# Kernel tuning notes

Measured on AMD Instinct MI355X. Metric: run time of the kernel, lower is better.

The kernel has to match this reference:

```python
import jax, jax.numpy as jnp
import numpy as np

R = 3.0            # search_range
EPS = 0.01         # forward_backward_error
UPD_MULT = 1.0     # UPDATE_MULTIPLIER_THRESHOLD


def _clamp(coords, H, W):
    # coords [..., 2] = (x, y); clamp x to [0, W-1], y to [0, H-1]
    return jnp.stack([jnp.clip(coords[..., 0], 0.0, W - 1.0),
                      jnp.clip(coords[..., 1], 0.0, H - 1.0)], axis=-1)


def _scores(coords, corr_flat):
    # coords [B,H,W,2] (x,y); corr_flat [B*H*W, Hc, Wc]; bilinear sample one scalar per pixel
    B, H, W, _ = coords.shape
    N, Hc, Wc = corr_flat.shape
    c = coords.reshape(-1, 2)
    x, y = c[:, 0], c[:, 1]
    x0 = jnp.floor(x); y0 = jnp.floor(y)
    wx = x - x0; wy = y - y0
    x0i = jnp.clip(x0.astype(jnp.int32), 0, Wc - 1)
    x1i = jnp.clip(x0i + 1, 0, Wc - 1)
    y0i = jnp.clip(y0.astype(jnp.int32), 0, Hc - 1)
    y1i = jnp.clip(y0i + 1, 0, Hc - 1)
    n = jnp.arange(N)
    v00 = corr_flat[n, y0i, x0i]; v01 = corr_flat[n, y0i, x1i]
    v10 = corr_flat[n, y1i, x0i]; v11 = corr_flat[n, y1i, x1i]
    s = (v00 * (1 - wx) * (1 - wy) + v01 * wx * (1 - wy)
         + v10 * (1 - wx) * wy + v11 * wx * wy)
    return s.reshape(B, H, W)


def _propagate(coords, corr_flat, dxy):
    # PatchMatch propagation step along direction (dx, dy): take neighbor's match
    # shifted by the same pixel offset if it scores higher.
    dx, dy = dxy
    B, H, W, _ = coords.shape
    best = coords
    best_s = _scores(best, corr_flat)
    cand_h = _clamp(jnp.roll(coords, dx, axis=2) + jnp.array([dx, 0.0], coords.dtype), H, W)
    cand_v = _clamp(jnp.roll(coords, dy, axis=1) + jnp.array([0.0, dy], coords.dtype), H, W)
    for cand in (cand_h, cand_v):
        s = _scores(cand, corr_flat)
        upd = s > best_s
        best = jnp.where(upd[..., None], cand, best)
        best_s = jnp.maximum(s, best_s)
    return best


def _random_search(coords, corr_flat, key):
    B, H, W, _ = coords.shape
    new = _clamp(coords + R * jax.random.normal(key, coords.shape, coords.dtype), H, W)
    old_s = _scores(coords, corr_flat)
    new_s = _scores(new, corr_flat)
    upd = (new_s - UPD_MULT * old_s) > 0
    return jnp.where(upd[..., None], new, coords)


def _handle(matching, corr_flat, key):
    coords = jnp.transpose(matching, (0, 2, 3, 1))  # [B,H,W,2]
    k1, k2, k3 = jax.random.split(key, 3)
    res = _propagate(coords, corr_flat, (1, 1))
    res = _random_search(res, corr_flat, k1)
    res = _propagate(res, corr_flat, (-1, -1))
    res = _random_search(res, corr_flat, k2)
    res = _propagate(res, corr_flat, (-1, 1))
    res = _random_search(res, corr_flat, k3)
    res = _propagate(res, corr_flat, (1, -1))
    return res


def _bilinear_map(img, coords):
    # img [B,H,W,C] sampled at coords [B,H,W,2] (x,y) -> [B,H,W,C]
    B, H, W, C = img.shape
    def per_b(im, co):
        x = co[..., 0].reshape(-1); y = co[..., 1].reshape(-1)
        x0 = jnp.floor(x); y0 = jnp.floor(y)
        wx = (x - x0)[:, None]; wy = (y - y0)[:, None]
        x0i = jnp.clip(x0.astype(jnp.int32), 0, W - 1)
        x1i = jnp.clip(x0i + 1, 0, W - 1)
        y0i = jnp.clip(y0.astype(jnp.int32), 0, H - 1)
        y1i = jnp.clip(y0i + 1, 0, H - 1)
        v00 = im[y0i, x0i]; v01 = im[y0i, x1i]
        v10 = im[y1i, x0i]; v11 = im[y1i, x1i]
        out = (v00 * (1 - wx) * (1 - wy) + v01 * wx * (1 - wy)
               + v10 * (1 - wx) * wy + v11 * wx * wy)
        return out.reshape(H, W, C)
    return jax.vmap(per_b)(img, coords)


def setup_inputs() -> dict:
    key = jax.random.key(0)
    k1, k2, k3 = jax.random.split(key, 3)
    B, H, W = 4, 64, 64
    # matching fields: absolute (x, y) coords in-range
    mf = jax.random.uniform(k1, (B, 2, H, W), jnp.float32)
    mb = jax.random.uniform(k2, (B, 2, H, W), jnp.float32)
    scale = jnp.array([W - 1.0, H - 1.0], jnp.float32).reshape(1, 2, 1, 1)
    matching_f = mf * scale
    matching_b = mb * scale
    corr_map = jax.random.normal(k3, (B, H, W, H, W), jnp.float32)
    return {"matching_f": matching_f, "matching_b": matching_b, "corr_map": corr_map}


def reference(matching_f, matching_b, corr_map):
    B, H, W = corr_map.shape[0], corr_map.shape[1], corr_map.shape[2]
    corr_f = corr_map.reshape(B * H * W, H, W)
    # backward direction samples the transposed correlation volume
    corr_b = jnp.transpose(corr_map, (0, 3, 4, 1, 2)).reshape(B * H * W, H, W)
    key = jax.random.key(42)
    kf, kb = jax.random.split(key)
    res_f = _handle(matching_f, corr_f, kf)   # [B,H,W,2]
    res_b = _handle(matching_b, corr_b, kb)   # [B,H,W,2]
    # forward-backward consistency: sample backward field at forward matches
    counter = _bilinear_map(res_b, res_f)
    diff = jnp.max(jnp.abs(res_f - counter), axis=-1)
    invalid = (diff > EPS)[..., None]
    res = jnp.where(invalid, jnp.transpose(matching_f, (0, 2, 3, 1)), res_f)
    return jnp.transpose(res, (0, 3, 1, 2))
```

## Files before the change

### kernel.cpp

```cpp
#include <hip/hip_runtime.h>
#include <stdint.h>

#pragma clang fp contract(off)

__host__ __device__ inline void tf2x32(uint32_t k0, uint32_t k1,
                                       uint32_t x0, uint32_t x1,
                                       uint32_t* o0, uint32_t* o1) {
  const uint32_t ks2 = k0 ^ k1 ^ 0x1BD11BDAu;
  x0 += k0; x1 += k1;
#define TF_R(r) { x0 += x1; x1 = (x1 << (r)) | (x1 >> (32 - (r))); x1 ^= x0; }
  TF_R(13) TF_R(15) TF_R(26) TF_R(6)
  x0 += k1;  x1 += ks2 + 1u;
  TF_R(17) TF_R(29) TF_R(16) TF_R(24)
  x0 += ks2; x1 += k0 + 2u;
  TF_R(13) TF_R(15) TF_R(26) TF_R(6)
  x0 += k0;  x1 += k1 + 3u;
  TF_R(17) TF_R(29) TF_R(16) TF_R(24)
  x0 += k1;  x1 += ks2 + 4u;
  TF_R(13) TF_R(15) TF_R(26) TF_R(6)
  x0 += ks2; x1 += k0 + 5u;
#undef TF_R
  *o0 = x0; *o1 = x1;
}

__device__ inline float erfinv_xla(float x) {
#pragma clang fp contract(off)
  float w = -log1pf(-(x * x));
  float p;
  if (w < 5.0f) {
    w = w - 2.5f;
    p = 2.81022636e-08f;
    p = 3.43273939e-07f  + p * w;
    p = -3.5233877e-06f  + p * w;
    p = -4.39150654e-06f + p * w;
    p = 0.00021858087f   + p * w;
    p = -0.00125372503f  + p * w;
    p = -0.00417768164f  + p * w;
    p = 0.246640727f     + p * w;
    p = 1.50140941f      + p * w;
  } else {
    w = sqrtf(w) - 3.0f;
    p = -0.000200214257f;
    p = 0.000100950558f  + p * w;
    p = 0.00134934322f   + p * w;
    p = -0.00367342844f  + p * w;
    p = 0.00573950773f   + p * w;
    p = -0.0076224613f   + p * w;
    p = 0.00943887047f   + p * w;
    p = 1.00167406f      + p * w;
    p = 2.83297682f      + p * w;
  }
  return p * x;
}

__device__ inline float jax_normal(uint32_t k0, uint32_t k1, uint32_t idx) {
#pragma clang fp contract(off)
  uint32_t o0, o1;
  tf2x32(k0, k1, 0u, idx, &o0, &o1);
  uint32_t bits = o0 ^ o1;
  float f = __uint_as_float((bits >> 9) | 0x3f800000u) - 1.0f;
  float u = f * 2.0f + (-0x1.fffffep-1f);
  u = fmaxf(-0x1.fffffep-1f, u);
  return 0x1.6a09e6p+0f * erfinv_xla(u);
}

__device__ inline float score_at(const float* __restrict__ base, int stride,
                                 float x, float y) {
#pragma clang fp contract(off)
  float x0 = floorf(x), y0 = floorf(y);
  float wx = x - x0, wy = y - y0;
  int xi = (int)x0; xi = xi < 0 ? 0 : (xi > 63 ? 63 : xi);
  int yi = (int)y0; yi = yi < 0 ? 0 : (yi > 63 ? 63 : yi);
  int x1 = xi + 1 > 63 ? 63 : xi + 1;
  int y1 = yi + 1 > 63 ? 63 : yi + 1;
  float v00 = base[(yi * 64 + xi) * stride];
  float v01 = base[(yi * 64 + x1) * stride];
  float v10 = base[(y1 * 64 + xi) * stride];
  float v11 = base[(y1 * 64 + x1) * stride];
  float omx = 1.0f - wx, omy = 1.0f - wy;
  return (((v00 * omx) * omy + (v01 * wx) * omy) + (v10 * omx) * wy) + (v11 * wx) * wy;
}

__global__ __launch_bounds__(64) void step_kernel(
    const float* __restrict__ mf, const float* __restrict__ mb,
    const float2* __restrict__ in_c, float2* __restrict__ out_c,
    const float* __restrict__ corr, int dx, int dy,
    uint32_t k0f, uint32_t k1f, uint32_t k0b, uint32_t k1b,
    int do_rs, int from_matching) {
#pragma clang fp contract(off)
  int g = (int)(blockIdx.x * 64 + threadIdx.x);
  int dir = g >> 14, b = (g >> 12) & 3, p = g & 4095;
  int i = p >> 6, j = p & 63;

  const float* base; int stride;
  if (dir == 0) { base = corr + (size_t)(b * 4096 + p) * 4096; stride = 1; }
  else          { base = corr + (size_t)b * 16777216 + p;      stride = 4096; }

  float2 c, ch, cv;
  int jh = (j - dx) & 63;
  int iv = (i - dy) & 63;
  if (from_matching) {
    const float* m = dir ? mb : mf;
    c  = make_float2(m[((b * 2 + 0) * 64 + i ) * 64 + j ], m[((b * 2 + 1) * 64 + i ) * 64 + j ]);
    ch = make_float2(m[((b * 2 + 0) * 64 + i ) * 64 + jh], m[((b * 2 + 1) * 64 + i ) * 64 + jh]);
    cv = make_float2(m[((b * 2 + 0) * 64 + iv) * 64 + j ], m[((b * 2 + 1) * 64 + iv) * 64 + j ]);
  } else {
    const float2* ic = in_c + dir * 16384 + b * 4096;
    c  = ic[p];
    ch = ic[(i << 6) | jh];
    cv = ic[(iv << 6) | j];
  }
  ch.x = fminf(fmaxf(ch.x + (float)dx, 0.0f), 63.0f);
  cv.y = fminf(fmaxf(cv.y + (float)dy, 0.0f), 63.0f);

  float s0 = score_at(base, stride, c.x,  c.y);
  float sh = score_at(base, stride, ch.x, ch.y);
  float sv = score_at(base, stride, cv.x, cv.y);
  float2 bst = c; float bs = s0;
  if (sh > bs) bst = ch;
  bs = fmaxf(sh, bs);
  if (sv > bs) bst = cv;
  bs = fmaxf(sv, bs);

  if (do_rs) {
    uint32_t kk0 = dir ? k0b : k0f, kk1 = dir ? k1b : k1f;
    uint32_t pg = (uint32_t)(b * 4096 + p);
    float n0 = jax_normal(kk0, kk1, 2u * pg);
    float n1 = jax_normal(kk0, kk1, 2u * pg + 1u);
    float nx = fminf(fmaxf(bst.x + 3.0f * n0, 0.0f), 63.0f);
    float ny = fminf(fmaxf(bst.y + 3.0f * n1, 0.0f), 63.0f);
    float sn = score_at(base, stride, nx, ny);
    if (sn - bs > 0.0f) bst = make_float2(nx, ny);
  }
  out_c[dir * 16384 + b * 4096 + p] = bst;
}

__global__ __launch_bounds__(256) void combine_kernel(const float* __restrict__ mf,
                                                      const float2* __restrict__ res,
                                                      float* __restrict__ out) {
#pragma clang fp contract(off)
  int pg = (int)(blockIdx.x * 256 + threadIdx.x);
  int b = pg >> 12, hw = pg & 4095;
  int i = hw >> 6, j = hw & 63;
  float2 rf = res[pg];
  const float2* rb = res + 16384 + b * 4096;
  float x0 = floorf(rf.x), y0 = floorf(rf.y);
  float wx = rf.x - x0, wy = rf.y - y0;
  int xi = (int)x0; xi = xi < 0 ? 0 : (xi > 63 ? 63 : xi);
  int yi = (int)y0; yi = yi < 0 ? 0 : (yi > 63 ? 63 : yi);
  int x1 = xi + 1 > 63 ? 63 : xi + 1;
  int y1 = yi + 1 > 63 ? 63 : yi + 1;
  float2 v00 = rb[yi * 64 + xi], v01 = rb[yi * 64 + x1];
  float2 v10 = rb[y1 * 64 + xi], v11 = rb[y1 * 64 + x1];
  float omx = 1.0f - wx, omy = 1.0f - wy;
  float c0 = (((v00.x * omx) * omy + (v01.x * wx) * omy) + (v10.x * omx) * wy) + (v11.x * wx) * wy;
  float c1 = (((v00.y * omx) * omy + (v01.y * wx) * omy) + (v10.y * omx) * wy) + (v11.y * wx) * wy;
  float d = fmaxf(fabsf(rf.x - c0), fabsf(rf.y - c1));
  bool invalid = d > 0.01f;
  out[((b * 2 + 0) * 64 + i) * 64 + j] = invalid ? mf[((b * 2 + 0) * 64 + i) * 64 + j] : rf.x;
  out[((b * 2 + 1) * 64 + i) * 64 + j] = invalid ? mf[((b * 2 + 1) * 64 + i) * 64 + j] : rf.y;
}

extern "C" void kernel_launch(void* const* d_in, const int* in_sizes, int n_in,
                              void* d_out, int out_size, void* d_ws, size_t ws_size,
                              hipStream_t stream) {
  const float* mf   = (const float*)d_in[0];
  const float* mb   = (const float*)d_in[1];
  const float* corr = (const float*)d_in[2];
  float* out  = (float*)d_out;
  float2* bufA = (float2*)d_ws;
  float2* bufB = bufA + 32768;

  uint32_t kf0, kf1, kb0, kb1, K[12];
  tf2x32(0u, 42u, 0u, 0u, &kf0, &kf1);
  tf2x32(0u, 42u, 0u, 1u, &kb0, &kb1);
  for (uint32_t s = 0; s < 3; ++s) {
    tf2x32(kf0, kf1, 0u, s, &K[0 + s * 2], &K[0 + s * 2 + 1]);
    tf2x32(kb0, kb1, 0u, s, &K[6 + s * 2], &K[6 + s * 2 + 1]);
  }

  dim3 grid(512), block(64);
  step_kernel<<<grid, block, 0, stream>>>(mf, mb, nullptr, bufA, corr,  1,  1,
                                          K[0], K[1], K[6], K[7], 1, 1);
  step_kernel<<<grid, block, 0, stream>>>(mf, mb, bufA, bufB, corr, -1, -1,
                                          K[2], K[3], K[8], K[9], 1, 0);
  step_kernel<<<grid, block, 0, stream>>>(mf, mb, bufB, bufA, corr, -1,  1,
                                          K[4], K[5], K[10], K[11], 1, 0);
  step_kernel<<<grid, block, 0, stream>>>(mf, mb, bufA, bufB, corr,  1, -1,
                                          0u, 0u, 0u, 0u, 0, 0);
  combine_kernel<<<dim3(64), dim3(256), 0, stream>>>(mf, bufB, out);
  (void)in_sizes; (void)n_in; (void)out_size; (void)ws_size;
}
```

Before: 334.4 us.

## Fuse PatchMatch steps and combine into one persistent kernel with grid barriers

Replaces the four step launches and the combine launch with a single persistent kernel. A software grid barrier (atomic counter plus spin) separates the steps, and each thread keeps its best coordinate and score in registers across steps. This removes per-launch overhead and the repeated gather that re-scored the current match at the start of each step. The random normals are computed once up front. In exchange it relies on all 512 blocks being resident at the same time, adds a memset for the barrier counters, and uses atomic loads and stores for the coordinate buffers.

```diff
diff --git a/kernel.cpp b/kernel.cpp
--- a/kernel.cpp
+++ b/kernel.cpp
@@ -2,6 +2,8 @@
 #include <stdint.h>
 
 #pragma clang fp contract(off)
+
+struct Keys { uint32_t k[12]; };
 
 __host__ __device__ inline void tf2x32(uint32_t k0, uint32_t k1,
                                        uint32_t x0, uint32_t x1,
@@ -81,38 +83,87 @@
   return (((v00 * omx) * omy + (v01 * wx) * omy) + (v10 * omx) * wy) + (v11 * wx) * wy;
 }
 
-__global__ __launch_bounds__(64) void step_kernel(
+__device__ __forceinline__ void st_coord(float2* buf, int idx, float2 v) {
+  unsigned long long u; __builtin_memcpy(&u, &v, 8);
+  __hip_atomic_store((unsigned long long*)(buf + idx), u,
+                     __ATOMIC_RELAXED, __HIP_MEMORY_SCOPE_AGENT);
+}
+__device__ __forceinline__ float2 ld_coord(const float2* buf, int idx) {
+  unsigned long long u = __hip_atomic_load((const unsigned long long*)(buf + idx),
+                                           __ATOMIC_RELAXED, __HIP_MEMORY_SCOPE_AGENT);
+  float2 v; __builtin_memcpy(&v, &u, 8); return v;
+}
+
+__device__ __forceinline__ void grid_barrier(uint32_t* bar, int slot, uint32_t nblk) {
+  __syncthreads();
+  if (threadIdx.x == 0) {
+    __threadfence();
+    atomicAdd(&bar[slot], 1u);
+    while (__hip_atomic_load(&bar[slot], __ATOMIC_RELAXED,
+                             __HIP_MEMORY_SCOPE_AGENT) < nblk)
+      __builtin_amdgcn_s_sleep(1);
+    __threadfence();
+  }
+  __syncthreads();
+}
+
+__device__ __forceinline__ void prop(const float2* buf, int gbase, int i, int j,
+                                     int dx, int dy, const float* __restrict__ base,
+                                     int stride, float2& bst, float& bs) {
+#pragma clang fp contract(off)
+  int jh = (j - dx) & 63;
+  int iv = (i - dy) & 63;
+  float2 ch = ld_coord(buf, gbase + ((i << 6) | jh));
+  float2 cv = ld_coord(buf, gbase + ((iv << 6) | j));
+  ch.x = fminf(fmaxf(ch.x + (float)dx, 0.0f), 63.0f);
+  cv.y = fminf(fmaxf(cv.y + (float)dy, 0.0f), 63.0f);
+  float sh = score_at(base, stride, ch.x, ch.y);
+  float sv = score_at(base, stride, cv.x, cv.y);
+  if (sh > bs) bst = ch;
+  bs = fmaxf(sh, bs);
+  if (sv > bs) bst = cv;
+  bs = fmaxf(sv, bs);
+}
+
+__device__ __forceinline__ void rs(const float* __restrict__ base, int stride,
+                                   float n0, float n1, float2& bst, float& bs) {
+#pragma clang fp contract(off)
+  float nx = fminf(fmaxf(bst.x + 3.0f * n0, 0.0f), 63.0f);
+  float ny = fminf(fmaxf(bst.y + 3.0f * n1, 0.0f), 63.0f);
+  float sn = score_at(base, stride, nx, ny);
+  if (sn - bs > 0.0f) { bst = make_float2(nx, ny); bs = sn; }
+}
+
+__global__ __launch_bounds__(64) void pm_all(
     const float* __restrict__ mf, const float* __restrict__ mb,
-    const float2* __restrict__ in_c, float2* __restrict__ out_c,
-    const float* __restrict__ corr, int dx, int dy,
-    uint32_t k0f, uint32_t k1f, uint32_t k0b, uint32_t k1b,
-    int do_rs, int from_matching) {
-#pragma clang fp contract(off)
-  int g = (int)(blockIdx.x * 64 + threadIdx.x);
-  int dir = g >> 14, b = (g >> 12) & 3, p = g & 4095;
-  int i = p >> 6, j = p & 63;
+    const float* __restrict__ corr, float* __restrict__ out,
+    float2* bufA, float2* bufB, uint32_t* bar, Keys keys) {
+#pragma clang fp contract(off)
+  const int g = (int)(blockIdx.x * 64 + threadIdx.x);
+  const int dir = g >> 14, b = (g >> 12) & 3, p = g & 4095;
+  const int i = p >> 6, j = p & 63;
+  const int gbase = g & ~4095;
+  const uint32_t nblk = gridDim.x;
 
   const float* base; int stride;
   if (dir == 0) { base = corr + (size_t)(b * 4096 + p) * 4096; stride = 1; }
   else          { base = corr + (size_t)b * 16777216 + p;      stride = 4096; }
 
-  float2 c, ch, cv;
-  int jh = (j - dx) & 63;
-  int iv = (i - dy) & 63;
-  if (from_matching) {
-    const float* m = dir ? mb : mf;
-    c  = make_float2(m[((b * 2 + 0) * 64 + i ) * 64 + j ], m[((b * 2 + 1) * 64 + i ) * 64 + j ]);
-    ch = make_float2(m[((b * 2 + 0) * 64 + i ) * 64 + jh], m[((b * 2 + 1) * 64 + i ) * 64 + jh]);
-    cv = make_float2(m[((b * 2 + 0) * 64 + iv) * 64 + j ], m[((b * 2 + 1) * 64 + iv) * 64 + j ]);
-  } else {
-    const float2* ic = in_c + dir * 16384 + b * 4096;
-    c  = ic[p];
-    ch = ic[(i << 6) | jh];
-    cv = ic[(iv << 6) | j];
-  }
-  ch.x = fminf(fmaxf(ch.x + (float)dx, 0.0f), 63.0f);
-  cv.y = fminf(fmaxf(cv.y + (float)dy, 0.0f), 63.0f);
-
+  const uint32_t* kk = &keys.k[dir * 6];
+  const uint32_t pg = (uint32_t)(b * 4096 + p);
+  float n[6];
+  for (int s = 0; s < 3; ++s) {
+    n[2 * s]     = jax_normal(kk[2 * s], kk[2 * s + 1], 2u * pg);
+    n[2 * s + 1] = jax_normal(kk[2 * s], kk[2 * s + 1], 2u * pg + 1u);
+  }
+
+  const float* m = dir ? mb : mf;
+  int jh = (j - 1) & 63, iv = (i - 1) & 63;
+  float2 c  = make_float2(m[((b * 2 + 0) * 64 + i ) * 64 + j ], m[((b * 2 + 1) * 64 + i ) * 64 + j ]);
+  float2 ch = make_float2(m[((b * 2 + 0) * 64 + i ) * 64 + jh], m[((b * 2 + 1) * 64 + i ) * 64 + jh]);
+  float2 cv = make_float2(m[((b * 2 + 0) * 64 + iv) * 64 + j ], m[((b * 2 + 1) * 64 + iv) * 64 + j ]);
+  ch.x = fminf(fmaxf(ch.x + 1.0f, 0.0f), 63.0f);
+  cv.y = fminf(fmaxf(cv.y + 1.0f, 0.0f), 63.0f);
   float s0 = score_at(base, stride, c.x,  c.y);
   float sh = score_at(base, stride, ch.x, ch.y);
   float sv = score_at(base, stride, cv.x, cv.y);
@@ -121,44 +172,45 @@
   bs = fmaxf(sh, bs);
   if (sv > bs) bst = cv;
   bs = fmaxf(sv, bs);
-
-  if (do_rs) {
-    uint32_t kk0 = dir ? k0b : k0f, kk1 = dir ? k1b : k1f;
-    uint32_t pg = (uint32_t)(b * 4096 + p);
-    float n0 = jax_normal(kk0, kk1, 2u * pg);
-    float n1 = jax_normal(kk0, kk1, 2u * pg + 1u);
-    float nx = fminf(fmaxf(bst.x + 3.0f * n0, 0.0f), 63.0f);
-    float ny = fminf(fmaxf(bst.y + 3.0f * n1, 0.0f), 63.0f);
-    float sn = score_at(base, stride, nx, ny);
-    if (sn - bs > 0.0f) bst = make_float2(nx, ny);
-  }
-  out_c[dir * 16384 + b * 4096 + p] = bst;
-}
-
-__global__ __launch_bounds__(256) void combine_kernel(const float* __restrict__ mf,
-                                                      const float2* __restrict__ res,
-                                                      float* __restrict__ out) {
-#pragma clang fp contract(off)
-  int pg = (int)(blockIdx.x * 256 + threadIdx.x);
-  int b = pg >> 12, hw = pg & 4095;
-  int i = hw >> 6, j = hw & 63;
-  float2 rf = res[pg];
-  const float2* rb = res + 16384 + b * 4096;
-  float x0 = floorf(rf.x), y0 = floorf(rf.y);
-  float wx = rf.x - x0, wy = rf.y - y0;
-  int xi = (int)x0; xi = xi < 0 ? 0 : (xi > 63 ? 63 : xi);
-  int yi = (int)y0; yi = yi < 0 ? 0 : (yi > 63 ? 63 : yi);
-  int x1 = xi + 1 > 63 ? 63 : xi + 1;
-  int y1 = yi + 1 > 63 ? 63 : yi + 1;
-  float2 v00 = rb[yi * 64 + xi], v01 = rb[yi * 64 + x1];
-  float2 v10 = rb[y1 * 64 + xi], v11 = rb[y1 * 64 + x1];
-  float omx = 1.0f - wx, omy = 1.0f - wy;
-  float c0 = (((v00.x * omx) * omy + (v01.x * wx) * omy) + (v10.x * omx) * wy) + (v11.x * wx) * wy;
-  float c1 = (((v00.y * omx) * omy + (v01.y * wx) * omy) + (v10.y * omx) * wy) + (v11.y * wx) * wy;
-  float d = fmaxf(fabsf(rf.x - c0), fabsf(rf.y - c1));
-  bool invalid = d > 0.01f;
-  out[((b * 2 + 0) * 64 + i) * 64 + j] = invalid ? mf[((b * 2 + 0) * 64 + i) * 64 + j] : rf.x;
-  out[((b * 2 + 1) * 64 + i) * 64 + j] = invalid ? mf[((b * 2 + 1) * 64 + i) * 64 + j] : rf.y;
+  rs(base, stride, n[0], n[1], bst, bs);
+  st_coord(bufA, g, bst);
+  grid_barrier(bar, 0, nblk);
+
+  prop(bufA, gbase, i, j, -1, -1, base, stride, bst, bs);
+  rs(base, stride, n[2], n[3], bst, bs);
+  st_coord(bufB, g, bst);
+  grid_barrier(bar, 1, nblk);
+
+  prop(bufB, gbase, i, j, -1, 1, base, stride, bst, bs);
+  rs(base, stride, n[4], n[5], bst, bs);
+  st_coord(bufA, g, bst);
+  grid_barrier(bar, 2, nblk);
+
+  prop(bufA, gbase, i, j, 1, -1, base, stride, bst, bs);
+  if (dir == 1) st_coord(bufB, g, bst);
+  grid_barrier(bar, 3, nblk);
+
+  if (dir == 0) {
+    float2 rf = bst;
+    const int rbb = 16384 + b * 4096;
+    float x0 = floorf(rf.x), y0 = floorf(rf.y);
+    float wx = rf.x - x0, wy = rf.y - y0;
+    int xi = (int)x0; xi = xi < 0 ? 0 : (xi > 63 ? 63 : xi);
+    int yi = (int)y0; yi = yi < 0 ? 0 : (yi > 63 ? 63 : yi);
+    int x1 = xi + 1 > 63 ? 63 : xi + 1;
+    int y1 = yi + 1 > 63 ? 63 : yi + 1;
+    float2 v00 = ld_coord(bufB, rbb + yi * 64 + xi);
+    float2 v01 = ld_coord(bufB, rbb + yi * 64 + x1);
+    float2 v10 = ld_coord(bufB, rbb + y1 * 64 + xi);
+    float2 v11 = ld_coord(bufB, rbb + y1 * 64 + x1);
+    float omx = 1.0f - wx, omy = 1.0f - wy;
+    float c0 = (((v00.x * omx) * omy + (v01.x * wx) * omy) + (v10.x * omx) * wy) + (v11.x * wx) * wy;
+    float c1 = (((v00.y * omx) * omy + (v01.y * wx) * omy) + (v10.y * omx) * wy) + (v11.y * wx) * wy;
+    float d = fmaxf(fabsf(rf.x - c0), fabsf(rf.y - c1));
+    bool invalid = d > 0.01f;
+    out[((b * 2 + 0) * 64 + i) * 64 + j] = invalid ? mf[((b * 2 + 0) * 64 + i) * 64 + j] : rf.x;
+    out[((b * 2 + 1) * 64 + i) * 64 + j] = invalid ? mf[((b * 2 + 1) * 64 + i) * 64 + j] : rf.y;
+  }
 }
 
 extern "C" void kernel_launch(void* const* d_in, const int* in_sizes, int n_in,
@@ -167,27 +219,22 @@
   const float* mf   = (const float*)d_in[0];
   const float* mb   = (const float*)d_in[1];
   const float* corr = (const float*)d_in[2];
-  float* out  = (float*)d_out;
-  float2* bufA = (float2*)d_ws;
-  float2* bufB = bufA + 32768;
-
-  uint32_t kf0, kf1, kb0, kb1, K[12];
+  float* out = (float*)d_out;
+
+  uint32_t* bar = (uint32_t*)d_ws;
+  float2* bufA  = (float2*)((char*)d_ws + 256);
+  float2* bufB  = bufA + 32768;
+
+  Keys K;
+  uint32_t kf0, kf1, kb0, kb1;
   tf2x32(0u, 42u, 0u, 0u, &kf0, &kf1);
   tf2x32(0u, 42u, 0u, 1u, &kb0, &kb1);
   for (uint32_t s = 0; s < 3; ++s) {
-    tf2x32(kf0, kf1, 0u, s, &K[0 + s * 2], &K[0 + s * 2 + 1]);
-    tf2x32(kb0, kb1, 0u, s, &K[6 + s * 2], &K[6 + s * 2 + 1]);
-  }
-
-  dim3 grid(512), block(64);
-  step_kernel<<<grid, block, 0, stream>>>(mf, mb, nullptr, bufA, corr,  1,  1,
-                                          K[0], K[1], K[6], K[7], 1, 1);
-  step_kernel<<<grid, block, 0, stream>>>(mf, mb, bufA, bufB, corr, -1, -1,
-                                          K[2], K[3], K[8], K[9], 1, 0);
-  step_kernel<<<grid, block, 0, stream>>>(mf, mb, bufB, bufA, corr, -1,  1,
-                                          K[4], K[5], K[10], K[11], 1, 0);
-  step_kernel<<<grid, block, 0, stream>>>(mf, mb, bufA, bufB, corr,  1, -1,
-                                          0u, 0u, 0u, 0u, 0, 0);
-  combine_kernel<<<dim3(64), dim3(256), 0, stream>>>(mf, bufB, out);
+    tf2x32(kf0, kf1, 0u, s, &K.k[0 + s * 2], &K.k[0 + s * 2 + 1]);
+    tf2x32(kb0, kb1, 0u, s, &K.k[6 + s * 2], &K.k[6 + s * 2 + 1]);
+  }
+
+  hipMemsetAsync(d_ws, 0, 256, stream);
+  pm_all<<<dim3(512), dim3(64), 0, stream>>>(mf, mb, corr, out, bufA, bufB, bar, K);
   (void)in_sizes; (void)n_in; (void)out_size; (void)ws_size;
 }
```

Measured after the change: 542.4 us. 1.62x slower.
